# Kernel optimization log

Hardware: AMD Instinct MI355X
Metric: run time of the kernel (lower is better)

The kernel has to match this reference:

```python
import jax, jax.numpy as jnp
import numpy as np

GRID = (32, 32)
LATENT = 256
ALPHA = 1.0
DECAY = 0.9


def _cdist(a, b):
    # Euclidean pairwise distance with a grad-safe sqrt (0 where d2==0, like torch.cdist).
    d2 = jnp.sum(a * a, -1)[:, None] + jnp.sum(b * b, -1)[None, :] - 2.0 * (a @ b.T)
    d2 = jnp.maximum(d2, 0.0)
    mask = d2 > 0
    return jnp.where(mask, jnp.sqrt(jnp.where(mask, d2, 1.0)), 0.0)


def setup_inputs() -> dict:
    key = jax.random.key(0)
    k1, k2 = jax.random.split(key)
    z = jax.random.normal(k1, (64, 512, 256), dtype=jnp.float32)
    nodes = jax.random.normal(k2, (GRID[0], GRID[1], LATENT), dtype=jnp.float32)
    return {"z": z, "nodes": nodes}


def reference(z, nodes):
    b, t, d = z.shape
    # time_decay^(seq_len - t - 1)
    tw = DECAY ** (t - 1 - jnp.arange(t, dtype=jnp.float32))
    z_flat = (z * tw[None, :, None]).reshape(b * t, d)   # (b t) d
    nodes_flat = nodes.reshape(-1, d)                     # n d

    dist = _cdist(z_flat, nodes_flat)                     # (b t) n
    q = 1.0 / (1.0 + dist / ALPHA) ** ((ALPHA + 1.0) / 2.0)
    q = q / jnp.sum(q, axis=-1, keepdims=True)            # L1 normalize rows
    q2 = q * q
    p = q2 / jnp.sum(q2, axis=0, keepdims=True)
    p = p / jnp.sum(p, axis=-1, keepdims=True)

    bmu = jnp.argmin(dist, axis=-1).reshape(b, t)         # int32

    # F.kl_div(q.log(), p, reduction='batchmean') = sum(p*(log p - log q)) / N
    kl_loss = jnp.sum(p * (jnp.log(p) - jnp.log(q))) / (b * t)
    diversity_loss = -jnp.mean(_cdist(nodes_flat, nodes_flat))
    time_smooth_loss = jnp.mean((z[:, 1:] - z[:, :-1]) ** 2) * DECAY

    # vectorized neighborhood consistency (python loop in the original is an
    # unweighted mean over all (b, t) adjacent pairs since seq_len is uniform)
    gw = GRID[1]
    pc = jnp.stack([bmu[:, :-1] // gw, bmu[:, :-1] % gw], axis=-1)
    nc = jnp.stack([bmu[:, 1:] // gw, bmu[:, 1:] % gw], axis=-1)
    neighbor_loss = jnp.mean(jnp.sum(jnp.abs(pc - nc), axis=-1).astype(jnp.float32))

    total_loss = kl_loss + 0.5 * diversity_loss + 0.3 * time_smooth_loss + 0.2 * neighbor_loss

    bmu_nodes = nodes_flat[bmu.reshape(-1)].reshape(b, t, d)
    som_z = z + 0.1 * (bmu_nodes - z)
    return (som_z, total_loss, kl_loss, diversity_loss, time_smooth_loss, neighbor_loss, q, bmu)
```

## Files before the change

### kernel.cpp

```cpp
#include <hip/hip_runtime.h>
#include <math.h>

#define Bb 64
#define Tt 512
#define Dd 256
#define Nn 1024
#define NROWS 32768

#define OUT_SOM 0L
#define OUT_SCAL 8388608L
#define OUT_Q 8388613L
#define OUT_BMU 41943045L

typedef __attribute__((ext_vector_type(8))) short bf16x8;
typedef __attribute__((ext_vector_type(4))) float f32x4;
typedef unsigned long long u64;
typedef unsigned short ushortT;

static __device__ __forceinline__ unsigned short f2bf(float x) {
  unsigned int u = __float_as_uint(x);
  unsigned int r = (u + 0x7fffu + ((u >> 16) & 1u)) >> 16;
  return (unsigned short)r;
}
static __device__ __forceinline__ float bf2f(unsigned short b) {
  return __uint_as_float(((unsigned int)b) << 16);
}

static __device__ __forceinline__ float block_reduce_sum(float v, float* sb) {
#pragma unroll
  for (int o = 32; o > 0; o >>= 1) v += __shfl_down(v, o, 64);
  const int lane = threadIdx.x & 63, w = threadIdx.x >> 6;
  if (lane == 0) sb[w] = v;
  __syncthreads();
  return (threadIdx.x == 0) ? (sb[0] + sb[1] + sb[2] + sb[3]) : 0.0f;
}

__global__ __launch_bounds__(256) void k_conv(
    const float* __restrict__ z, const float* __restrict__ nodes,
    ushortT* __restrict__ zhiF, ushortT* __restrict__ zloF, float* __restrict__ zn,
    ushortT* __restrict__ nhiF, ushortT* __restrict__ nloF, float* __restrict__ nnorm) {
  __shared__ float sm[32 * 260];
  const int tid = threadIdx.x;
  if (blockIdx.x < 1024) {
    const int rt = blockIdx.x;
    const long row0 = (long)rt * 32;
    const int r = tid >> 3, c8 = tid & 7;
    const long rowg = row0 + r;
    const int t = (int)(rowg & (Tt - 1));
    const float tw = powf(0.9f, (float)(Tt - 1 - t));
    float nrm = 0.f;
#pragma unroll
    for (int k = 0; k < 8; ++k) {
      const int c4 = c8 + k * 8;
      float4 v = ((const float4*)(z + rowg * Dd))[c4];
      v.x *= tw; v.y *= tw; v.z *= tw; v.w *= tw;
      *(float4*)&sm[r * 260 + c4 * 4] = v;
      nrm += v.x * v.x + v.y * v.y + v.z * v.z + v.w * v.w;
    }
    nrm += __shfl_xor(nrm, 1, 64);
    nrm += __shfl_xor(nrm, 2, 64);
    nrm += __shfl_xor(nrm, 4, 64);
    if (c8 == 0) zn[rowg] = nrm;
    __syncthreads();
    ushort4* oh = (ushort4*)(zhiF + (long)rt * 8192);
    ushort4* ol = (ushort4*)(zloF + (long)rt * 8192);
#pragma unroll
    for (int i = 0; i < 8; ++i) {
      const int o4 = tid + 256 * i;
      const int e4 = (o4 & 1) * 4;
      const int r16 = (o4 >> 1) & 15;
      const int k8 = (o4 >> 5) & 3;
      const int g = (o4 >> 7) & 1;
      const int ks = o4 >> 8;
      const float* p = &sm[(g * 16 + r16) * 260 + ks * 32 + k8 * 8 + e4];
      const float4 v = *(const float4*)p;
      ushort4 h, l;
      h.x = f2bf(v.x); l.x = f2bf(v.x - bf2f(h.x));
      h.y = f2bf(v.y); l.y = f2bf(v.y - bf2f(h.y));
      h.z = f2bf(v.z); l.z = f2bf(v.z - bf2f(h.z));
      h.w = f2bf(v.w); l.w = f2bf(v.w - bf2f(h.w));
      oh[o4] = h;
      ol[o4] = l;
    }
  } else {
    const int ct = blockIdx.x - 1024;
    const int jr = tid >> 4, cg = tid & 15;
    const long nrow = (long)(ct * 16 + jr);
    float nrm = 0.f;
#pragma unroll
    for (int k = 0; k < 4; ++k) {
      const int c4 = cg + k * 16;
      const float4 v = ((const float4*)(nodes + nrow * Dd))[c4];
      *(float4*)&sm[jr * 260 + c4 * 4] = v;
      nrm += v.x * v.x + v.y * v.y + v.z * v.z + v.w * v.w;
    }
    nrm += __shfl_xor(nrm, 1, 64);
    nrm += __shfl_xor(nrm, 2, 64);
    nrm += __shfl_xor(nrm, 4, 64);
    nrm += __shfl_xor(nrm, 8, 64);
    if (cg == 0) nnorm[nrow] = nrm;
    __syncthreads();
    ushort4* oh = (ushort4*)(nhiF + (long)ct * 4096);
    ushort4* ol = (ushort4*)(nloF + (long)ct * 4096);
#pragma unroll
    for (int i = 0; i < 4; ++i) {
      const int o4 = tid + 256 * i;
      const int e4 = (o4 & 1) * 4;
      const int c16 = (o4 >> 1) & 15;
      const int k8 = (o4 >> 5) & 3;
      const int ks = o4 >> 7;
      const float* p = &sm[c16 * 260 + ks * 32 + k8 * 8 + e4];
      const float4 v = *(const float4*)p;
      ushort4 h, l;
      h.x = f2bf(v.x); l.x = f2bf(v.x - bf2f(h.x));
      h.y = f2bf(v.y); l.y = f2bf(v.y - bf2f(h.y));
      h.z = f2bf(v.z); l.z = f2bf(v.z - bf2f(h.z));
      h.w = f2bf(v.w); l.w = f2bf(v.w - bf2f(h.w));
      oh[o4] = h;
      ol[o4] = l;
    }
  }
}

__global__ __launch_bounds__(512) void k_gemm2(
    const ushortT* __restrict__ zhiF, const ushortT* __restrict__ zloF,
    const ushortT* __restrict__ nhiF, const ushortT* __restrict__ nloF,
    const float* __restrict__ zn, const float* __restrict__ nn,
    float* __restrict__ qout, float* __restrict__ bmuf, float* __restrict__ colsum) {
  __shared__ float srowS[32][8];
  __shared__ u64 sbmu[32][8];
  __shared__ float sinv[32];
  const int tid = threadIdx.x, lane = tid & 63, w = tid >> 6;
  const int rl = lane & 15, kq = lane >> 4;
  const int rt = blockIdx.x;
  const long row0 = (long)rt * 32;

  const ushortT* Ah = zhiF + (long)rt * 8192;
  const ushortT* Al = zloF + (long)rt * 8192;
  const ushortT* Bh = nhiF + (long)w * 8 * 4096;
  const ushortT* Bl = nloF + (long)w * 8 * 4096;
  const int lo8 = lane * 8;

  f32x4 acc[2][8];
#pragma unroll
  for (int g = 0; g < 2; ++g)
#pragma unroll
    for (int c = 0; c < 8; ++c) acc[g][c] = (f32x4){0.f, 0.f, 0.f, 0.f};

#pragma unroll 1
  for (int ks = 0; ks < 8; ++ks) {
    const bf16x8 ah0 = *(const bf16x8*)(Ah + (ks * 2 + 0) * 512 + lo8);
    const bf16x8 ah1 = *(const bf16x8*)(Ah + (ks * 2 + 1) * 512 + lo8);
    const bf16x8 al0 = *(const bf16x8*)(Al + (ks * 2 + 0) * 512 + lo8);
    const bf16x8 al1 = *(const bf16x8*)(Al + (ks * 2 + 1) * 512 + lo8);
#pragma unroll
    for (int c = 0; c < 8; ++c) {
      const bf16x8 bh = *(const bf16x8*)(Bh + c * 4096 + ks * 512 + lo8);
      const bf16x8 bl = *(const bf16x8*)(Bl + c * 4096 + ks * 512 + lo8);
      acc[0][c] = __builtin_amdgcn_mfma_f32_16x16x32_bf16(ah0, bh, acc[0][c], 0, 0, 0);
      acc[0][c] = __builtin_amdgcn_mfma_f32_16x16x32_bf16(ah0, bl, acc[0][c], 0, 0, 0);
      acc[0][c] = __builtin_amdgcn_mfma_f32_16x16x32_bf16(al0, bh, acc[0][c], 0, 0, 0);
      acc[1][c] = __builtin_amdgcn_mfma_f32_16x16x32_bf16(ah1, bh, acc[1][c], 0, 0, 0);
      acc[1][c] = __builtin_amdgcn_mfma_f32_16x16x32_bf16(ah1, bl, acc[1][c], 0, 0, 0);
      acc[1][c] = __builtin_amdgcn_mfma_f32_16x16x32_bf16(al1, bh, acc[1][c], 0, 0, 0);
    }
  }

  float znv[2][4], nnv[8];
#pragma unroll
  for (int g = 0; g < 2; ++g)
#pragma unroll
    for (int r = 0; r < 4; ++r) znv[g][r] = zn[row0 + g * 16 + kq * 4 + r];
#pragma unroll
  for (int c = 0; c < 8; ++c) nnv[c] = nn[w * 128 + c * 16 + rl];

  float rs[2][4];
  u64 bm[2][4];
#pragma unroll
  for (int g = 0; g < 2; ++g)
#pragma unroll
    for (int r = 0; r < 4; ++r) { rs[g][r] = 0.f; bm[g][r] = ~0ull; }

#pragma unroll
  for (int g = 0; g < 2; ++g)
#pragma unroll
    for (int c = 0; c < 8; ++c)
#pragma unroll
      for (int r = 0; r < 4; ++r) {
        const float dot = acc[g][c][r];
        const float d2 = znv[g][r] + nnv[c] - 2.f * dot;
        const float dist = sqrtf(fmaxf(d2, 0.f));
        const float qv = 1.f / (1.f + dist);
        acc[g][c][r] = qv;
        rs[g][r] += qv;
        const int col = w * 128 + c * 16 + rl;
        const u64 pk = ((u64)__float_as_uint(dist) << 32) | (unsigned int)col;
        bm[g][r] = pk < bm[g][r] ? pk : bm[g][r];
      }
#pragma unroll
  for (int g = 0; g < 2; ++g)
#pragma unroll
    for (int r = 0; r < 4; ++r) {
#pragma unroll
      for (int m = 1; m < 16; m <<= 1) {
        rs[g][r] += __shfl_xor(rs[g][r], m, 64);
        const u64 o = __shfl_xor(bm[g][r], m, 64);
        bm[g][r] = o < bm[g][r] ? o : bm[g][r];
      }
      if (rl == 0) {
        srowS[g * 16 + kq * 4 + r][w] = rs[g][r];
        sbmu[g * 16 + kq * 4 + r][w] = bm[g][r];
      }
    }
  __syncthreads();
  if (tid < 32) {
    float s = 0.f;
    u64 best = ~0ull;
#pragma unroll
    for (int i = 0; i < 8; ++i) {
      s += srowS[tid][i];
      const u64 v = sbmu[tid][i];
      best = v < best ? v : best;
    }
    sinv[tid] = 1.f / s;
    bmuf[row0 + tid] = (float)(int)(unsigned int)(best & 0xffffffffull);
  }
  __syncthreads();

  float inv[2][4];
#pragma unroll
  for (int g = 0; g < 2; ++g)
#pragma unroll
    for (int r = 0; r < 4; ++r) inv[g][r] = sinv[g * 16 + kq * 4 + r];

  float cp[8];
#pragma unroll
  for (int c = 0; c < 8; ++c) cp[c] = 0.f;
#pragma unroll
  for (int g = 0; g < 2; ++g)
#pragma unroll
    for (int c = 0; c < 8; ++c)
#pragma unroll
      for (int r = 0; r < 4; ++r) {
        const float qn = acc[g][c][r] * inv[g][r];
        qout[(row0 + g * 16 + kq * 4 + r) * Nn + w * 128 + c * 16 + rl] = qn;
        cp[c] = fmaf(qn, qn, cp[c]);
      }
#pragma unroll
  for (int c = 0; c < 8; ++c) {
    cp[c] += __shfl_xor(cp[c], 16, 64);
    cp[c] += __shfl_xor(cp[c], 32, 64);
    if (kq == 0) atomicAdd(&colsum[w * 128 + c * 16 + rl], cp[c]);
  }
}

__global__ __launch_bounds__(256) void k_div2(
    const ushortT* __restrict__ nhiF, const ushortT* __restrict__ nloF,
    const float* __restrict__ nnorm, float* __restrict__ scal) {
  __shared__ float sb[4];
  const int tid = threadIdx.x, lane = tid & 63, w = tid >> 6;
  const int rl = lane & 15, kq = lane >> 4;
  const int bi = blockIdx.x;
  const int lo8 = lane * 8;

  f32x4 acc[16];
#pragma unroll
  for (int c = 0; c < 16; ++c) acc[c] = (f32x4){0.f, 0.f, 0.f, 0.f};

#pragma unroll 1
  for (int ks = 0; ks < 8; ++ks) {
    const bf16x8 ah = *(const bf16x8*)(nhiF + (long)bi * 4096 + ks * 512 + lo8);
    const bf16x8 al = *(const bf16x8*)(nloF + (long)bi * 4096 + ks * 512 + lo8);
#pragma unroll
    for (int c = 0; c < 16; ++c) {
      const long ct = (long)(w * 16 + c);
      const bf16x8 bh = *(const bf16x8*)(nhiF + ct * 4096 + ks * 512 + lo8);
      const bf16x8 bl = *(const bf16x8*)(nloF + ct * 4096 + ks * 512 + lo8);
      acc[c] = __builtin_amdgcn_mfma_f32_16x16x32_bf16(ah, bh, acc[c], 0, 0, 0);
      acc[c] = __builtin_amdgcn_mfma_f32_16x16x32_bf16(ah, bl, acc[c], 0, 0, 0);
      acc[c] = __builtin_amdgcn_mfma_f32_16x16x32_bf16(al, bh, acc[c], 0, 0, 0);
    }
  }
  float ni[4];
#pragma unroll
  for (int r = 0; r < 4; ++r) ni[r] = nnorm[bi * 16 + kq * 4 + r];
  float dsum = 0.f;
#pragma unroll
  for (int c = 0; c < 16; ++c) {
    const float nj = nnorm[w * 256 + c * 16 + rl];
#pragma unroll
    for (int r = 0; r < 4; ++r) {
      const float d2 = ni[r] + nj - 2.f * acc[c][r];
      dsum += sqrtf(fmaxf(d2, 0.f));
    }
  }
  const float tot = block_reduce_sum(dsum, sb);
  if (tid == 0) atomicAdd(&scal[1], tot);
}

__global__ __launch_bounds__(256) void k_kl(const float* __restrict__ q,
                                            const float* __restrict__ colsum,
                                            float* __restrict__ scal) {
  __shared__ float rcs[Nn];
  __shared__ float lcs[Nn];
  __shared__ float sb[4];
  const int tid = threadIdx.x, lane = tid & 63, wave = tid >> 6;
#pragma unroll
  for (int j = 0; j < 4; ++j) {
    const float cs = colsum[tid + 256 * j];
    rcs[tid + 256 * j] = 1.f / cs;
    lcs[tid + 256 * j] = __logf(cs);
  }
  __syncthreads();
  const long r0 = (long)blockIdx.x * 16;
  float klp = 0.f;
  for (int rr = 0; rr < 4; ++rr) {
    const long row = r0 + rr * 4 + wave;
    float s = 0.f, a = 0.f;
#pragma unroll
    for (int j = 0; j < 16; ++j) {
      const int col = lane + 64 * j;
      const float t = q[row * Nn + col];
      const float u = t * t * rcs[col];
      s += u;
      a = fmaf(u, __logf(t) - lcs[col], a);
    }
#pragma unroll
    for (int o = 1; o < 64; o <<= 1) {
      s += __shfl_xor(s, o, 64);
      a += __shfl_xor(a, o, 64);
    }
    if (lane == 0) klp += a / s - __logf(s);
  }
  const float tot = block_reduce_sum(klp, sb);
  if (tid == 0) atomicAdd(&scal[0], tot);
}

__global__ __launch_bounds__(256) void k_somnb(const float* __restrict__ z,
                                               const float* __restrict__ nodes,
                                               const float* __restrict__ bmuf,
                                               float* __restrict__ som,
                                               float* __restrict__ scal) {
  __shared__ float sb[4];
  const int tid = threadIdx.x;
  const long r0 = (long)blockIdx.x * 16;
  float ts = 0.f, zp = 0.f;
  if ((r0 & (Tt - 1)) > 0) zp = z[(r0 - 1) * Dd + tid];
  for (int r = 0; r < 16; ++r) {
    const long row = r0 + r;
    const float zc = z[row * Dd + tid];
    const int bi = (int)bmuf[row];
    const float nv = nodes[(long)bi * Dd + tid];
    som[row * Dd + tid] = zc + 0.1f * (nv - zc);
    if ((row & (Tt - 1)) > 0) {
      const float dd = zc - zp;
      ts = fmaf(dd, dd, ts);
    }
    zp = zc;
  }
  const float tts = block_reduce_sum(ts, sb);
  if (tid == 0) atomicAdd(&scal[2], tts);
  float nbv = 0.f;
  if (tid < 16) {
    const long row = r0 + tid;
    if ((row & (Tt - 1)) != (Tt - 1)) {
      const int b1 = (int)bmuf[row], b2 = (int)bmuf[row + 1];
      nbv = (float)(abs((b1 >> 5) - (b2 >> 5)) + abs((b1 & 31) - (b2 & 31)));
    }
  }
  __syncthreads();
  const float tnb = block_reduce_sum(nbv, sb);
  if (tid == 0) atomicAdd(&scal[3], tnb);
}

__global__ void k_final(const float* __restrict__ scal, float* __restrict__ o) {
  const float kl = scal[0] * (1.f / 32768.f);
  const float dv = -scal[1] * (1.f / (1024.f * 1024.f));
  const float ts = scal[2] * (0.9f / (64.f * 511.f * 256.f));
  const float nb = scal[3] * (1.f / 32704.f);
  o[0] = kl + 0.5f * dv + 0.3f * ts + 0.2f * nb;
  o[1] = kl;
  o[2] = dv;
  o[3] = ts;
  o[4] = nb;
}

__global__ __launch_bounds__(256) void k_prep_fb(const float* __restrict__ nodes,
                                                 float* __restrict__ nt,
                                                 float* __restrict__ nnorm) {
  __shared__ float sb[4];
  const int j = blockIdx.x, d = threadIdx.x;
  const float v = nodes[j * Dd + d];
  nt[(long)d * Nn + j] = v;
  const float tot = block_reduce_sum(v * v, sb);
  if (threadIdx.x == 0) nnorm[j] = tot;
}

__global__ __launch_bounds__(256) void k_div_fb(const float* __restrict__ nodes,
                                                const float* __restrict__ nt,
                                                const float* __restrict__ nnorm,
                                                float* __restrict__ scal) {
  __shared__ float ni[4][Dd];
  __shared__ float sb[4];
  const int tid = threadIdx.x;
  const int i0 = blockIdx.x * 4;
#pragma unroll
  for (int r = 0; r < 4; ++r) ni[r][tid] = nodes[(i0 + r) * Dd + tid];
  __syncthreads();
  float acc[4][4];
#pragma unroll
  for (int r = 0; r < 4; ++r)
#pragma unroll
    for (int jj = 0; jj < 4; ++jj) acc[r][jj] = 0.f;
  for (int d = 0; d < Dd; ++d) {
    float nj[4];
#pragma unroll
    for (int jj = 0; jj < 4; ++jj) nj[jj] = nt[(long)d * Nn + tid + 256 * jj];
#pragma unroll
    for (int r = 0; r < 4; ++r) {
      const float s = ni[r][d];
#pragma unroll
      for (int jj = 0; jj < 4; ++jj) acc[r][jj] = fmaf(s, nj[jj], acc[r][jj]);
    }
  }
  float sum = 0.f;
#pragma unroll
  for (int r = 0; r < 4; ++r)
#pragma unroll
    for (int jj = 0; jj < 4; ++jj) {
      const float d2 = nnorm[i0 + r] + nnorm[tid + 256 * jj] - 2.f * acc[r][jj];
      sum += sqrtf(fmaxf(d2, 0.f));
    }
  const float tot = block_reduce_sum(sum, sb);
  if (tid == 0) atomicAdd(&scal[1], tot);
}

__global__ __launch_bounds__(256) void k_dist_fb(
    const float* __restrict__ z, const float* __restrict__ nt,
    const float* __restrict__ nnorm, float* __restrict__ qout,
    float* __restrict__ srow, float* __restrict__ bmuf) {
  __shared__ float zt[Dd][65];
  __shared__ float rs4[4][64];
  __shared__ u64 cand[4][64];
  const int tid = threadIdx.x, lane = tid & 63, wave = tid >> 6;
  const long row0 = (long)blockIdx.x * 64;
  for (int k = 0; k < 64; ++k) {
    const int t = (int)((row0 + k) & (Tt - 1));
    const float tw = powf(0.9f, (float)(Tt - 1 - t));
    zt[tid][k] = z[(row0 + k) * Dd + tid] * tw;
  }
  __syncthreads();
  float zns = 0.f;
  for (int d = 0; d < Dd; ++d) {
    const float v = zt[d][lane];
    zns = fmaf(v, v, zns);
  }
  const long myrow = row0 + lane;
  float rsum = 0.f;
  u64 best = ~0ull;
  const int j0w = wave * 256;
  for (int chunk = 0; chunk < 16; ++chunk) {
    const int j0 = j0w + chunk * 16;
    float acc[16];
#pragma unroll
    for (int i = 0; i < 16; ++i) acc[i] = 0.f;
    const float* ntp = nt + j0;
    for (int d = 0; d < Dd; ++d) {
      const float zv = zt[d][lane];
      const float4 a = ((const float4*)ntp)[0];
      const float4 b = ((const float4*)ntp)[1];
      const float4 c = ((const float4*)ntp)[2];
      const float4 e = ((const float4*)ntp)[3];
      ntp += Nn;
      acc[0] = fmaf(zv, a.x, acc[0]); acc[1] = fmaf(zv, a.y, acc[1]);
      acc[2] = fmaf(zv, a.z, acc[2]); acc[3] = fmaf(zv, a.w, acc[3]);
      acc[4] = fmaf(zv, b.x, acc[4]); acc[5] = fmaf(zv, b.y, acc[5]);
      acc[6] = fmaf(zv, b.z, acc[6]); acc[7] = fmaf(zv, b.w, acc[7]);
      acc[8] = fmaf(zv, c.x, acc[8]); acc[9] = fmaf(zv, c.y, acc[9]);
      acc[10] = fmaf(zv, c.z, acc[10]); acc[11] = fmaf(zv, c.w, acc[11]);
      acc[12] = fmaf(zv, e.x, acc[12]); acc[13] = fmaf(zv, e.y, acc[13]);
      acc[14] = fmaf(zv, e.z, acc[14]); acc[15] = fmaf(zv, e.w, acc[15]);
    }
#pragma unroll
    for (int jj = 0; jj < 16; ++jj) {
      const int j = j0 + jj;
      const float d2 = zns + nnorm[j] - 2.f * acc[jj];
      const float dist = sqrtf(fmaxf(d2, 0.f));
      const float qr = 1.f / (1.f + dist);
      qout[myrow * Nn + j] = qr;
      rsum += qr;
      const u64 pk = ((u64)__float_as_uint(dist) << 32) | (unsigned int)j;
      best = pk < best ? pk : best;
    }
  }
  rs4[wave][lane] = rsum;
  cand[wave][lane] = best;
  __syncthreads();
  if (wave == 0) {
    const float s = rs4[0][lane] + rs4[1][lane] + rs4[2][lane] + rs4[3][lane];
    srow[myrow] = s;
    const u64 m0 = cand[0][lane] < cand[1][lane] ? cand[0][lane] : cand[1][lane];
    const u64 m1 = cand[2][lane] < cand[3][lane] ? cand[2][lane] : cand[3][lane];
    const u64 m = m0 < m1 ? m0 : m1;
    bmuf[myrow] = (float)(int)(unsigned int)(m & 0xffffffffull);
  }
}

__global__ __launch_bounds__(256) void k_norm_fb(float* __restrict__ q,
                                                 const float* __restrict__ srow,
                                                 float* __restrict__ colsum) {
  const int tid = threadIdx.x;
  const long r0 = (long)blockIdx.x * 16;
  float cs[4] = {0.f, 0.f, 0.f, 0.f};
  for (int r = 0; r < 16; ++r) {
    const long row = r0 + r;
    const float inv = 1.f / srow[row];
#pragma unroll
    for (int j = 0; j < 4; ++j) {
      const long idx = row * Nn + tid + 256 * j;
      const float v = q[idx] * inv;
      q[idx] = v;
      cs[j] = fmaf(v, v, cs[j]);
    }
  }
#pragma unroll
  for (int j = 0; j < 4; ++j) atomicAdd(&colsum[tid + 256 * j], cs[j]);
}

extern "C" void kernel_launch(void* const* d_in, const int* in_sizes, int n_in,
                              void* d_out, int out_size, void* d_ws, size_t ws_size,
                              hipStream_t stream) {
  const float* z = (const float*)d_in[0];
  const float* nodes = (const float*)d_in[1];
  float* out = (float*)d_out;
  unsigned char* ws = (unsigned char*)d_ws;

  float* som = out + OUT_SOM;
  float* scal_out = out + OUT_SCAL;
  float* qout = out + OUT_Q;
  float* bmuf = out + OUT_BMU;

  const size_t NEED = 34742288;
  if (ws_size >= NEED) {
    ushortT* zhiF = (ushortT*)(ws + 0);
    ushortT* zloF = (ushortT*)(ws + 16777216);
    ushortT* nhiF = (ushortT*)(ws + 33554432);
    ushortT* nloF = (ushortT*)(ws + 34078720);
    float* zn = (float*)(ws + 34603008);
    float* nnorm = (float*)(ws + 34734080);
    float* colsum = (float*)(ws + 34738176);
    float* scal = (float*)(ws + 34742272);

    hipMemsetAsync(colsum, 0, 4096 + 16, stream);

    k_conv<<<1088, 256, 0, stream>>>(z, nodes, zhiF, zloF, zn, nhiF, nloF, nnorm);
    k_gemm2<<<1024, 512, 0, stream>>>(zhiF, zloF, nhiF, nloF, zn, nnorm, qout, bmuf, colsum);
    k_div2<<<64, 256, 0, stream>>>(nhiF, nloF, nnorm, scal);
    k_kl<<<2048, 256, 0, stream>>>(qout, colsum, scal);
    k_somnb<<<2048, 256, 0, stream>>>(z, nodes, bmuf, som, scal);
    k_final<<<1, 1, 0, stream>>>(scal, scal_out);
  } else {
    float* wsf = (float*)ws;
    float* nt = wsf;
    float* nnorm = wsf + 262144;
    float* srow = wsf + 263168;
    float* colsum = wsf + 295936;
    float* scal = wsf + 296960;

    hipMemsetAsync(colsum, 0, (1024 + 4) * sizeof(float), stream);
    k_prep_fb<<<1024, 256, 0, stream>>>(nodes, nt, nnorm);
    k_div_fb<<<256, 256, 0, stream>>>(nodes, nt, nnorm, scal);
    k_dist_fb<<<512, 256, 0, stream>>>(z, nt, nnorm, qout, srow, bmuf);
    k_norm_fb<<<2048, 256, 0, stream>>>(qout, srow, colsum);
    k_kl<<<2048, 256, 0, stream>>>(qout, colsum, scal);
    k_somnb<<<2048, 256, 0, stream>>>(z, nodes, bmuf, som, scal);
    k_final<<<1, 1, 0, stream>>>(scal, scal_out);
  }
}
```

Baseline: 277.5 us.

## Double GEMM row tile to reuse node fragments and split diversity kernel wider

```diff
diff --git a/kernel.cpp b/kernel.cpp
--- a/kernel.cpp
+++ b/kernel.cpp
@@ -122,98 +122,112 @@
   }
 }
 
-__global__ __launch_bounds__(512) void k_gemm2(
+__global__ __launch_bounds__(512, 2) void k_gemm3(
     const ushortT* __restrict__ zhiF, const ushortT* __restrict__ zloF,
     const ushortT* __restrict__ nhiF, const ushortT* __restrict__ nloF,
     const float* __restrict__ zn, const float* __restrict__ nn,
     float* __restrict__ qout, float* __restrict__ bmuf, float* __restrict__ colsum) {
-  __shared__ float srowS[32][8];
-  __shared__ u64 sbmu[32][8];
-  __shared__ float sinv[32];
+  __shared__ float srowS[64][8];
+  __shared__ u64 sbmu[64][8];
+  __shared__ float sinv[64];
   const int tid = threadIdx.x, lane = tid & 63, w = tid >> 6;
   const int rl = lane & 15, kq = lane >> 4;
-  const int rt = blockIdx.x;
-  const long row0 = (long)rt * 32;
-
-  const ushortT* Ah = zhiF + (long)rt * 8192;
-  const ushortT* Al = zloF + (long)rt * 8192;
+  const long row0 = (long)blockIdx.x * 64;
+
+  const ushortT* Ah0 = zhiF + (long)blockIdx.x * 16384;
+  const ushortT* Al0 = zloF + (long)blockIdx.x * 16384;
   const ushortT* Bh = nhiF + (long)w * 8 * 4096;
   const ushortT* Bl = nloF + (long)w * 8 * 4096;
   const int lo8 = lane * 8;
 
-  f32x4 acc[2][8];
-#pragma unroll
-  for (int g = 0; g < 2; ++g)
-#pragma unroll
-    for (int c = 0; c < 8; ++c) acc[g][c] = (f32x4){0.f, 0.f, 0.f, 0.f};
+  f32x4 acc[2][2][8];
+#pragma unroll
+  for (int rg = 0; rg < 2; ++rg)
+#pragma unroll
+    for (int g = 0; g < 2; ++g)
+#pragma unroll
+      for (int c = 0; c < 8; ++c) acc[rg][g][c] = (f32x4){0.f, 0.f, 0.f, 0.f};
 
 #pragma unroll 1
   for (int ks = 0; ks < 8; ++ks) {
-    const bf16x8 ah0 = *(const bf16x8*)(Ah + (ks * 2 + 0) * 512 + lo8);
-    const bf16x8 ah1 = *(const bf16x8*)(Ah + (ks * 2 + 1) * 512 + lo8);
-    const bf16x8 al0 = *(const bf16x8*)(Al + (ks * 2 + 0) * 512 + lo8);
-    const bf16x8 al1 = *(const bf16x8*)(Al + (ks * 2 + 1) * 512 + lo8);
+    bf16x8 ah[2][2], al[2][2];
+#pragma unroll
+    for (int rg = 0; rg < 2; ++rg)
+#pragma unroll
+      for (int g = 0; g < 2; ++g) {
+        ah[rg][g] = *(const bf16x8*)(Ah0 + rg * 8192 + (ks * 2 + g) * 512 + lo8);
+        al[rg][g] = *(const bf16x8*)(Al0 + rg * 8192 + (ks * 2 + g) * 512 + lo8);
+      }
 #pragma unroll
     for (int c = 0; c < 8; ++c) {
       const bf16x8 bh = *(const bf16x8*)(Bh + c * 4096 + ks * 512 + lo8);
       const bf16x8 bl = *(const bf16x8*)(Bl + c * 4096 + ks * 512 + lo8);
-      acc[0][c] = __builtin_amdgcn_mfma_f32_16x16x32_bf16(ah0, bh, acc[0][c], 0, 0, 0);
-      acc[0][c] = __builtin_amdgcn_mfma_f32_16x16x32_bf16(ah0, bl, acc[0][c], 0, 0, 0);
-      acc[0][c] = __builtin_amdgcn_mfma_f32_16x16x32_bf16(al0, bh, acc[0][c], 0, 0, 0);
-      acc[1][c] = __builtin_amdgcn_mfma_f32_16x16x32_bf16(ah1, bh, acc[1][c], 0, 0, 0);
-      acc[1][c] = __builtin_amdgcn_mfma_f32_16x16x32_bf16(ah1, bl, acc[1][c], 0, 0, 0);
-      acc[1][c] = __builtin_amdgcn_mfma_f32_16x16x32_bf16(al1, bh, acc[1][c], 0, 0, 0);
-    }
-  }
-
-  float znv[2][4], nnv[8];
-#pragma unroll
-  for (int g = 0; g < 2; ++g)
-#pragma unroll
-    for (int r = 0; r < 4; ++r) znv[g][r] = zn[row0 + g * 16 + kq * 4 + r];
+      __builtin_amdgcn_s_setprio(1);
+#pragma unroll
+      for (int rg = 0; rg < 2; ++rg)
+#pragma unroll
+        for (int g = 0; g < 2; ++g) {
+          acc[rg][g][c] = __builtin_amdgcn_mfma_f32_16x16x32_bf16(ah[rg][g], bh, acc[rg][g][c], 0, 0, 0);
+          acc[rg][g][c] = __builtin_amdgcn_mfma_f32_16x16x32_bf16(ah[rg][g], bl, acc[rg][g][c], 0, 0, 0);
+          acc[rg][g][c] = __builtin_amdgcn_mfma_f32_16x16x32_bf16(al[rg][g], bh, acc[rg][g][c], 0, 0, 0);
+        }
+      __builtin_amdgcn_s_setprio(0);
+    }
+  }
+
+  float nnv[8];
 #pragma unroll
   for (int c = 0; c < 8; ++c) nnv[c] = nn[w * 128 + c * 16 + rl];
 
-  float rs[2][4];
-  u64 bm[2][4];
-#pragma unroll
-  for (int g = 0; g < 2; ++g)
-#pragma unroll
-    for (int r = 0; r < 4; ++r) { rs[g][r] = 0.f; bm[g][r] = ~0ull; }
-
-#pragma unroll
-  for (int g = 0; g < 2; ++g)
-#pragma unroll
-    for (int c = 0; c < 8; ++c)
+#pragma unroll
+  for (int rg = 0; rg < 2; ++rg) {
+    float rs[2][4];
+    u64 bm[2][4];
+#pragma unroll
+    for (int g = 0; g < 2; ++g)
 #pragma unroll
       for (int r = 0; r < 4; ++r) {
-        const float dot = acc[g][c][r];
-        const float d2 = znv[g][r] + nnv[c] - 2.f * dot;
-        const float dist = sqrtf(fmaxf(d2, 0.f));
-        const float qv = 1.f / (1.f + dist);
-        acc[g][c][r] = qv;
-        rs[g][r] += qv;
-        const int col = w * 128 + c * 16 + rl;
-        const u64 pk = ((u64)__float_as_uint(dist) << 32) | (unsigned int)col;
-        bm[g][r] = pk < bm[g][r] ? pk : bm[g][r];
+        rs[g][r] = 0.f;
+        bm[g][r] = ~0ull;
       }
 #pragma unroll
-  for (int g = 0; g < 2; ++g)
-#pragma unroll
-    for (int r = 0; r < 4; ++r) {
-#pragma unroll
-      for (int m = 1; m < 16; m <<= 1) {
-        rs[g][r] += __shfl_xor(rs[g][r], m, 64);
-        const u64 o = __shfl_xor(bm[g][r], m, 64);
-        bm[g][r] = o < bm[g][r] ? o : bm[g][r];
+    for (int g = 0; g < 2; ++g) {
+      float znv[4];
+#pragma unroll
+      for (int r = 0; r < 4; ++r) znv[r] = zn[row0 + rg * 32 + g * 16 + kq * 4 + r];
+#pragma unroll
+      for (int c = 0; c < 8; ++c)
+#pragma unroll
+        for (int r = 0; r < 4; ++r) {
+          const float dot = acc[rg][g][c][r];
+          const float d2 = znv[r] + nnv[c] - 2.f * dot;
+          const float dist = sqrtf(fmaxf(d2, 0.f));
+          const float qv = 1.f / (1.f + dist);
+          acc[rg][g][c][r] = qv;
+          rs[g][r] += qv;
+          const int col = w * 128 + c * 16 + rl;
+          const u64 pk = ((u64)__float_as_uint(dist) << 32) | (unsigned int)col;
+          bm[g][r] = pk < bm[g][r] ? pk : bm[g][r];
+        }
+    }
+#pragma unroll
+    for (int g = 0; g < 2; ++g)
+#pragma unroll
+      for (int r = 0; r < 4; ++r) {
+#pragma unroll
+        for (int m = 1; m < 16; m <<= 1) {
+          rs[g][r] += __shfl_xor(rs[g][r], m, 64);
+          const u64 o = __shfl_xor(bm[g][r], m, 64);
+          bm[g][r] = o < bm[g][r] ? o : bm[g][r];
+        }
+        if (rl == 0) {
+          srowS[rg * 32 + g * 16 + kq * 4 + r][w] = rs[g][r];
+          sbmu[rg * 32 + g * 16 + kq * 4 + r][w] = bm[g][r];
+        }
       }
-      if (rl == 0) {
-        srowS[g * 16 + kq * 4 + r][w] = rs[g][r];
-        sbmu[g * 16 + kq * 4 + r][w] = bm[g][r];
-      }
-    }
-  __syncthreads();
-  if (tid < 32) {
+  }
+  __syncthreads();
+  if (tid < 64) {
     float s = 0.f;
     u64 best = ~0ull;
 #pragma unroll
@@ -227,25 +241,25 @@
   }
   __syncthreads();
 
-  float inv[2][4];
-#pragma unroll
-  for (int g = 0; g < 2; ++g)
-#pragma unroll
-    for (int r = 0; r < 4; ++r) inv[g][r] = sinv[g * 16 + kq * 4 + r];
-
   float cp[8];
 #pragma unroll
   for (int c = 0; c < 8; ++c) cp[c] = 0.f;
 #pragma unroll
-  for (int g = 0; g < 2; ++g)
-#pragma unroll
-    for (int c = 0; c < 8; ++c)
-#pragma unroll
-      for (int r = 0; r < 4; ++r) {
-        const float qn = acc[g][c][r] * inv[g][r];
-        qout[(row0 + g * 16 + kq * 4 + r) * Nn + w * 128 + c * 16 + rl] = qn;
-        cp[c] = fmaf(qn, qn, cp[c]);
-      }
+  for (int rg = 0; rg < 2; ++rg)
+#pragma unroll
+    for (int g = 0; g < 2; ++g) {
+      float inv[4];
+#pragma unroll
+      for (int r = 0; r < 4; ++r) inv[r] = sinv[rg * 32 + g * 16 + kq * 4 + r];
+#pragma unroll
+      for (int c = 0; c < 8; ++c)
+#pragma unroll
+        for (int r = 0; r < 4; ++r) {
+          const float qn = acc[rg][g][c][r] * inv[r];
+          qout[(row0 + rg * 32 + g * 16 + kq * 4 + r) * Nn + w * 128 + c * 16 + rl] = qn;
+          cp[c] = fmaf(qn, qn, cp[c]);
+        }
+    }
 #pragma unroll
   for (int c = 0; c < 8; ++c) {
     cp[c] += __shfl_xor(cp[c], 16, 64);
@@ -260,20 +274,21 @@
   __shared__ float sb[4];
   const int tid = threadIdx.x, lane = tid & 63, w = tid >> 6;
   const int rl = lane & 15, kq = lane >> 4;
-  const int bi = blockIdx.x;
+  const int bi = blockIdx.x & 63;
+  const int cq = blockIdx.x >> 6;
   const int lo8 = lane * 8;
 
-  f32x4 acc[16];
-#pragma unroll
-  for (int c = 0; c < 16; ++c) acc[c] = (f32x4){0.f, 0.f, 0.f, 0.f};
+  f32x4 acc[4];
+#pragma unroll
+  for (int c = 0; c < 4; ++c) acc[c] = (f32x4){0.f, 0.f, 0.f, 0.f};
 
 #pragma unroll 1
   for (int ks = 0; ks < 8; ++ks) {
     const bf16x8 ah = *(const bf16x8*)(nhiF + (long)bi * 4096 + ks * 512 + lo8);
     const bf16x8 al = *(const bf16x8*)(nloF + (long)bi * 4096 + ks * 512 + lo8);
 #pragma unroll
-    for (int c = 0; c < 16; ++c) {
-      const long ct = (long)(w * 16 + c);
+    for (int c = 0; c < 4; ++c) {
+      const long ct = (long)(cq * 16 + w * 4 + c);
       const bf16x8 bh = *(const bf16x8*)(nhiF + ct * 4096 + ks * 512 + lo8);
       const bf16x8 bl = *(const bf16x8*)(nloF + ct * 4096 + ks * 512 + lo8);
       acc[c] = __builtin_amdgcn_mfma_f32_16x16x32_bf16(ah, bh, acc[c], 0, 0, 0);
@@ -286,8 +301,8 @@
   for (int r = 0; r < 4; ++r) ni[r] = nnorm[bi * 16 + kq * 4 + r];
   float dsum = 0.f;
 #pragma unroll
-  for (int c = 0; c < 16; ++c) {
-    const float nj = nnorm[w * 256 + c * 16 + rl];
+  for (int c = 0; c < 4; ++c) {
+    const float nj = nnorm[(cq * 16 + w * 4 + c) * 16 + rl];
 #pragma unroll
     for (int r = 0; r < 4; ++r) {
       const float d2 = ni[r] + nj - 2.f * acc[c][r];
@@ -554,8 +569,8 @@
     hipMemsetAsync(colsum, 0, 4096 + 16, stream);
 
     k_conv<<<1088, 256, 0, stream>>>(z, nodes, zhiF, zloF, zn, nhiF, nloF, nnorm);
-    k_gemm2<<<1024, 512, 0, stream>>>(zhiF, zloF, nhiF, nloF, zn, nnorm, qout, bmuf, colsum);
-    k_div2<<<64, 256, 0, stream>>>(nhiF, nloF, nnorm, scal);
+    k_gemm3<<<512, 512, 0, stream>>>(zhiF, zloF, nhiF, nloF, zn, nnorm, qout, bmuf, colsum);
+    k_div2<<<256, 256, 0, stream>>>(nhiF, nloF, nnorm, scal);
     k_kl<<<2048, 256, 0, stream>>>(qout, colsum, scal);
     k_somnb<<<2048, 256, 0, stream>>>(z, nodes, bmuf, som, scal);
     k_final<<<1, 1, 0, stream>>>(scal, scal_out);
```

After: 249.9 us. 10.0% less time.
